# Performance work log

Hardware: AMD Instinct MI355X
Metric: run time of the kernel (lower is better)

## Reference

```python
import jax, jax.numpy as jnp
import numpy as np

B, L, D, F, K, M = 32, 1024, 384, 384, 3, 4096
LN_EPS = 1e-5


def setup_inputs() -> dict:
    key = jax.random.key(0)
    ks = jax.random.split(key, 6)
    w = lambda k, shp: jax.random.normal(k, shp, jnp.float32) * 0.02
    return {
        "x": jax.random.normal(ks[0], (B, L, D), jnp.float32),
        "target": jax.random.randint(ks[1], (B, L), 0, 5),
        "mel_max_length": M,
        "conv1_w": w(ks[2], (F, D, K)),  # OIW layout
        "conv1_b": jnp.zeros((F,), jnp.float32),
        "ln1_g": jnp.ones((F,), jnp.float32),
        "ln1_b": jnp.zeros((F,), jnp.float32),
        "conv2_w": w(ks[3], (F, F, K)),
        "conv2_b": jnp.zeros((F,), jnp.float32),
        "ln2_g": jnp.ones((F,), jnp.float32),
        "ln2_b": jnp.zeros((F,), jnp.float32),
        "lin_w": w(ks[4], (F, 1)),
        "lin_b": jnp.zeros((1,), jnp.float32),
    }


def conv1d_same(x, w, b):
    # x: [B, L, C], w: [O, I, K] -> [B, L, O], 'same' padding
    pad = (w.shape[-1] - 1) // 2
    y = jax.lax.conv_general_dilated(
        x, w, window_strides=(1,), padding=[(pad, pad)],
        dimension_numbers=("NWC", "OIW", "NWC"))
    return y + b


def layernorm(x, g, b):
    m = jnp.mean(x, axis=-1, keepdims=True)
    v = jnp.mean(jnp.square(x - m), axis=-1, keepdims=True)
    return (x - m) * jax.lax.rsqrt(v + LN_EPS) * g + b


def duration_predictor(x, c1w, c1b, g1, b1, c2w, c2b, g2, b2, lw, lb):
    h = jnp.maximum(layernorm(conv1d_same(x, c1w, c1b), g1, b1), 0.0)
    h = jnp.maximum(layernorm(conv1d_same(h, c2w, c2b), g2, b2), 0.0)
    return jnp.maximum(h @ lw + lb, 0.0)[..., 0]  # [B, L]


def length_regulate(x, durations, mel_max_length):
    # Equivalent to one-hot alignment matmul + zero pad, done as a gather.
    cum = jnp.cumsum(durations, axis=1)  # [B, L]
    t = jnp.arange(mel_max_length)       # [M]
    # frame t belongs to phoneme j where cum[j-1] <= t < cum[j]
    idx = jax.vmap(lambda c: jnp.searchsorted(c, t, side="right"))(cum)  # [B, M]
    valid = (t[None, :] < cum[:, -1:]).astype(x.dtype)                    # [B, M]
    idx = jnp.minimum(idx, durations.shape[1] - 1)
    out = jnp.take_along_axis(x, idx[..., None], axis=1) * valid[..., None]
    return out  # [B, M, D]


def reference(x, target, mel_max_length, conv1_w, conv1_b, ln1_g, ln1_b,
              conv2_w, conv2_b, ln2_g, ln2_b, lin_w, lin_b):
    dur_pred = duration_predictor(x, conv1_w, conv1_b, ln1_g, ln1_b,
                                  conv2_w, conv2_b, ln2_g, ln2_b, lin_w, lin_b)
    out = length_regulate(x, target, mel_max_length)
    return out, dur_pred
```

## Files before the change

kernel.cpp:

```cpp
#include <hip/hip_runtime.h>

#define DEV __device__ __forceinline__

typedef unsigned short u16;
typedef __attribute__((ext_vector_type(8))) short bf16x8;
typedef __attribute__((ext_vector_type(8))) unsigned short u16x8;
typedef __attribute__((ext_vector_type(4))) float f32x4;

constexpr int Bz = 32, Lz = 1024, Dz = 384, Fz = 384, KWz = 3, Mz = 4096;
constexpr float EPS = 1e-5f;

DEV u16 f2bf(float f) {
  unsigned u = __float_as_uint(f);
  u += 0x7fffu + ((u >> 16) & 1u);
  return (u16)(u >> 16);
}

typedef __attribute__((address_space(1))) const unsigned char ga_t;
typedef __attribute__((address_space(3))) unsigned char la_t;
DEV void gload16(const void* g, void* l) {
  __builtin_amdgcn_global_load_lds((ga_t*)g, (la_t*)l, 16, 0, 0);
}

__global__ void k_pre(const float* __restrict__ x, u16* __restrict__ xbf,
                      const float* __restrict__ w1, const float* __restrict__ w2,
                      u16* __restrict__ w1t, u16* __restrict__ w2t,
                      u16* __restrict__ h1) {
  constexpr int CONV_BLKS = (Bz * Lz * Dz / 8) / 256;
  if (blockIdx.x < CONV_BLKS) {
    int gid = blockIdx.x * 256 + threadIdx.x;
    size_t e = (size_t)gid * 8;
    float4 v0 = *reinterpret_cast<const float4*>(x + e);
    float4 v1 = *reinterpret_cast<const float4*>(x + e + 4);
    int d = (int)(e % Dz);
    int l = (int)((e / Dz) % Lz);
    int b = (int)(e / ((size_t)Dz * Lz));
    u16x8 u;
    u[0] = f2bf(v0.x); u[1] = f2bf(v0.y); u[2] = f2bf(v0.z); u[3] = f2bf(v0.w);
    u[4] = f2bf(v1.x); u[5] = f2bf(v1.y); u[6] = f2bf(v1.z); u[7] = f2bf(v1.w);
    *reinterpret_cast<u16x8*>(xbf + ((size_t)(b * (Lz + 2) + l + 1)) * Dz + d) = u;
    return;
  }
  int gid = (blockIdx.x - CONV_BLKS) * 256 + threadIdx.x;
  constexpr int WT = KWz * Fz * Dz;
  if (gid < WT) {
    int k = gid / (Fz * Dz), rem = gid % (Fz * Dz);
    int f = rem / Dz, d = rem % Dz;
    w1t[gid] = f2bf(w1[(f * Dz + d) * KWz + k]);
  } else if (gid < 2 * WT) {
    int g2 = gid - WT;
    int k = g2 / (Fz * Fz), rem = g2 % (Fz * Fz);
    int co = rem / Fz, ci = rem % Fz;
    w2t[g2] = f2bf(w2[(co * Fz + ci) * KWz + k]);
  } else {
    int p = gid - 2 * WT;
    if (p < 2 * Bz * 2 * Dz) {
      u16* buf = (p < Bz * 2 * Dz) ? xbf : h1;
      int q = p % (Bz * 2 * Dz);
      int b = q / (2 * Dz), r = (q / Dz) & 1, d = q % Dz;
      size_t row = (size_t)b * (Lz + 2) + (r ? (Lz + 1) : 0);
      buf[row * Dz + d] = 0;
    }
  }
}

__global__ __launch_bounds__(1024) void k_scan(const int* __restrict__ tgt,
                                               int* __restrict__ idxb) {
  __shared__ int sc[Lz];
  int b = blockIdx.x, tid = threadIdx.x;
  sc[tid] = tgt[b * Lz + tid];
  __syncthreads();
  for (int off = 1; off < Lz; off <<= 1) {
    int add = (tid >= off) ? sc[tid - off] : 0;
    __syncthreads();
    sc[tid] += add;
    __syncthreads();
  }
  int total = sc[Lz - 1];
  for (int t = tid; t < Mz; t += 1024) {
    int lo = 0, hi = Lz;
    while (lo < hi) {
      int mid = (lo + hi) >> 1;
      if (sc[mid] > t) hi = mid; else lo = mid + 1;
    }
    int iv = (t < total) ? (lo > Lz - 1 ? Lz - 1 : lo) : -1;
    idxb[b * Mz + t] = iv;
  }
}

__global__ void k_gather(const float* __restrict__ x, const int* __restrict__ idxb,
                         float* __restrict__ out) {
  int wid = (blockIdx.x * blockDim.x + threadIdx.x) >> 6;
  int lane = threadIdx.x & 63;
  int nw = (gridDim.x * blockDim.x) >> 6;
  for (int row = wid; row < Bz * Mz; row += nw) {
    int b = row >> 12;
    int iv = idxb[row];
    float4* dst = reinterpret_cast<float4*>(out + (size_t)row * Dz);
    if (iv < 0) {
      float4 z = make_float4(0.f, 0.f, 0.f, 0.f);
      dst[lane] = z;
      if (lane < 32) dst[64 + lane] = z;
    } else {
      const float4* src =
          reinterpret_cast<const float4*>(x + ((size_t)b * Lz + iv) * Dz);
      dst[lane] = src[lane];
      if (lane < 32) dst[64 + lane] = src[64 + lane];
    }
  }
}

template <int LAYER>
__global__ __launch_bounds__(512, 2) void k_conv(
    const u16* __restrict__ in,
    const u16* __restrict__ wt,
    const float* __restrict__ cbias,
    const float* __restrict__ lng, const float* __restrict__ lnb,
    u16* __restrict__ hout,
    const float* __restrict__ lw, const float* __restrict__ lbias,
    float* __restrict__ dur)
{
  __shared__ __align__(16) u16 Ash[3][128 * 32];
  __shared__ __align__(16) u16 Bsh[3][384 * 32];
  __shared__ float s_sum[4][128], s_sq[4][128], s_dot[4][128];

  const int tid = threadIdx.x;
  const int lane = tid & 63, wave = tid >> 6;
  const int wr = wave >> 2, wc = wave & 3;
  const int l15 = lane & 15, lh = lane >> 4;
  const int b = blockIdx.x >> 3, l0 = (blockIdx.x & 7) << 7;

  const u16* in_row = in + ((size_t)(b * (Lz + 2) + l0)) * 384;
  int gof[4], ldo[4];
  bool isa[4];
  #pragma unroll
  for (int i = 0; i < 4; ++i) {
    int c = wave + 8 * i;
    bool a = (c < 8);
    int cb = a ? c : c - 8;
    int slot = cb * 64 + lane, r = slot >> 2, q = slot & 3;
    int ks = q ^ ((r >> 1) & 3);
    gof[i] = r * 384 + ks * 8;
    ldo[i] = cb * 512;
    isa[i] = a;
  }

  auto STAGE = [&](int kt, int buf) {
    int tap = kt / 12;
    int d0 = (kt - tap * 12) * 32;
    const u16* sa = in_row + tap * 384 + d0;
    const u16* sb = wt + tap * (384 * 384) + d0;
    #pragma unroll
    for (int i = 0; i < 4; ++i) {
      if (isa[i]) gload16(sa + gof[i], &Ash[buf][ldo[i]]);
      else        gload16(sb + gof[i], &Bsh[buf][ldo[i]]);
    }
  };

  int aoff[4], boff[6];
  #pragma unroll
  for (int m = 0; m < 4; ++m) {
    int r = wr * 64 + m * 16 + l15;
    aoff[m] = r * 32 + (lh ^ ((r >> 1) & 3)) * 8;
  }
  #pragma unroll
  for (int n = 0; n < 6; ++n) {
    int c = wc * 96 + n * 16 + l15;
    boff[n] = c * 32 + (lh ^ ((c >> 1) & 3)) * 8;
  }

  f32x4 acc[4][6] = {};

  STAGE(0, 0);
  STAGE(1, 1);
  int cur = 0;
  for (int kt = 0; kt < 36; ++kt) {
    if (kt < 35) asm volatile("s_waitcnt vmcnt(4)" ::: "memory");
    else         asm volatile("s_waitcnt vmcnt(0)" ::: "memory");
    __builtin_amdgcn_s_barrier();
    __builtin_amdgcn_sched_barrier(0);
    bf16x8 av[4], bv[6];
    #pragma unroll
    for (int m = 0; m < 4; ++m)
      av[m] = *reinterpret_cast<const bf16x8*>(&Ash[cur][aoff[m]]);
    #pragma unroll
    for (int n = 0; n < 6; ++n)
      bv[n] = *reinterpret_cast<const bf16x8*>(&Bsh[cur][boff[n]]);
    if (kt < 34) {
      int nb = cur + 2; if (nb >= 3) nb -= 3;
      STAGE(kt + 2, nb);
    }
    #pragma unroll
    for (int m = 0; m < 4; ++m)
      #pragma unroll
      for (int n = 0; n < 6; ++n)
        acc[m][n] =
            __builtin_amdgcn_mfma_f32_16x16x32_bf16(av[m], bv[n], acc[m][n], 0, 0, 0);
    cur = (cur == 2) ? 0 : cur + 1;
  }

  __syncthreads();
  float gv[6], bvv[6], cbv[6], lwv[6];
  #pragma unroll
  for (int n = 0; n < 6; ++n) {
    int c = wc * 96 + n * 16 + l15;
    gv[n] = lng[c]; bvv[n] = lnb[c]; cbv[n] = cbias[c];
    lwv[n] = (LAYER == 2) ? lw[c] : 0.f;
  }
  #pragma unroll
  for (int m = 0; m < 4; ++m) {
    #pragma unroll
    for (int r = 0; r < 4; ++r) {
      float s = 0.f, q2 = 0.f;
      #pragma unroll
      for (int n = 0; n < 6; ++n) {
        float v = acc[m][n][r] + cbv[n];
        s += v; q2 += v * v;
      }
      #pragma unroll
      for (int off = 1; off < 16; off <<= 1) {
        s += __shfl_xor(s, off);
        q2 += __shfl_xor(q2, off);
      }
      if (l15 == 0) {
        int row = wr * 64 + m * 16 + lh * 4 + r;
        s_sum[wc][row] = s;
        s_sq[wc][row] = q2;
      }
    }
  }
  __syncthreads();
  #pragma unroll
  for (int m = 0; m < 4; ++m) {
    #pragma unroll
    for (int r = 0; r < 4; ++r) {
      int row = wr * 64 + m * 16 + lh * 4 + r;
      float S = 0.f, Q = 0.f;
      #pragma unroll
      for (int w = 0; w < 4; ++w) { S += s_sum[w][row]; Q += s_sq[w][row]; }
      float mean = S * (1.f / 384.f);
      float var = Q * (1.f / 384.f) - mean * mean;
      float rstd = rsqrtf(var + EPS);
      float dotp = 0.f;
      #pragma unroll
      for (int n = 0; n < 6; ++n) {
        float v = acc[m][n][r] + cbv[n];
        float y = fmaxf((v - mean) * rstd * gv[n] + bvv[n], 0.f);
        if constexpr (LAYER == 1) {
          int c = wc * 96 + n * 16 + l15;
          hout[((size_t)(b * (Lz + 2) + l0 + row + 1)) * 384 + c] = f2bf(y);
        } else {
          dotp += y * lwv[n];
        }
      }
      if constexpr (LAYER == 2) {
        #pragma unroll
        for (int off = 1; off < 16; off <<= 1) dotp += __shfl_xor(dotp, off);
        if (l15 == 0) s_dot[wc][row] = dotp;
      }
    }
  }
  if constexpr (LAYER == 2) {
    __syncthreads();
    if (tid < 128) {
      float dsum = lbias[0];
      #pragma unroll
      for (int w = 0; w < 4; ++w) dsum += s_dot[w][tid];
      dur[(size_t)b * Lz + l0 + tid] = fmaxf(dsum, 0.f);
    }
  }
}

extern "C" void kernel_launch(void* const* d_in, const int* in_sizes, int n_in,
                              void* d_out, int out_size, void* d_ws, size_t ws_size,
                              hipStream_t stream) {
  (void)in_sizes; (void)n_in; (void)out_size; (void)ws_size;
  const float* x   = (const float*)d_in[0];
  const int* tgt   = (const int*)d_in[1];
  const float* w1  = (const float*)d_in[3];
  const float* c1b = (const float*)d_in[4];
  const float* g1  = (const float*)d_in[5];
  const float* b1  = (const float*)d_in[6];
  const float* w2  = (const float*)d_in[7];
  const float* c2b = (const float*)d_in[8];
  const float* g2  = (const float*)d_in[9];
  const float* b2  = (const float*)d_in[10];
  const float* lw  = (const float*)d_in[11];
  const float* lb  = (const float*)d_in[12];

  float* out0 = (float*)d_out;
  float* dur  = out0 + (size_t)Bz * Mz * Dz;

  const size_t xbf_n = (size_t)Bz * (Lz + 2) * Dz;
  const size_t wt_n  = (size_t)KWz * Fz * Dz;
  u16* xbf = (u16*)d_ws;
  u16* h1  = xbf + xbf_n;
  u16* w1t = h1 + xbf_n;
  u16* w2t = w1t + wt_n;
  int* idxb = (int*)(w2t + wt_n);

  constexpr int CONV_BLKS = (Bz * Lz * Dz / 8) / 256;
  constexpr int PREP_BLKS = (2 * KWz * Fz * Dz + 2 * Bz * 2 * Dz + 255) / 256;
  k_pre<<<CONV_BLKS + PREP_BLKS, 256, 0, stream>>>(x, xbf, w1, w2, w1t, w2t, h1);
  k_scan<<<Bz, 1024, 0, stream>>>(tgt, idxb);
  k_conv<1><<<256, 512, 0, stream>>>(xbf, w1t, c1b, g1, b1, h1, nullptr, nullptr,
                                     nullptr);
  k_conv<2><<<256, 512, 0, stream>>>(h1, w2t, c2b, g2, b2, nullptr, lw, lb, dur);
  k_gather<<<2048, 256, 0, stream>>>(x, idxb, out0);
}
```

Measured before the change: 134.6 us.

## Fuse scan into prep kernel and overlap gather with conv via extra waves

Merges the cumsum/searchsorted scan into the preprocessing kernel as extra blocks and removes the standalone gather kernel. Each conv block gets four extra waves that copy half of the length-regulated output rows while the MFMA waves compute, matching their barriers to the conv's K-loop. The intent is to hide the memory-bound gather behind the compute-bound convolutions and cut launch count. The risk is that the extra waves and barrier matching alter occupancy (launch bounds 768,3), and any barrier-count mismatch with the unseen conv loop would hang or corrupt results.

```diff
diff --git a/kernel.cpp b/kernel.cpp
--- a/kernel.cpp
+++ b/kernel.cpp
@@ -22,13 +22,20 @@
   __builtin_amdgcn_global_load_lds((ga_t*)g, (la_t*)l, 16, 0, 0);
 }
 
-__global__ void k_pre(const float* __restrict__ x, u16* __restrict__ xbf,
-                      const float* __restrict__ w1, const float* __restrict__ w2,
-                      u16* __restrict__ w1t, u16* __restrict__ w2t,
-                      u16* __restrict__ h1) {
-  constexpr int CONV_BLKS = (Bz * Lz * Dz / 8) / 256;
+__global__ __launch_bounds__(1024) void k_pre(
+    const float* __restrict__ x, u16* __restrict__ xbf,
+    const float* __restrict__ w1, const float* __restrict__ w2,
+    u16* __restrict__ w1t, u16* __restrict__ w2t, u16* __restrict__ h1,
+    const int* __restrict__ tgt, int* __restrict__ idxb) {
+  __shared__ int sc[Lz];
+  constexpr int CONV_BLKS = (Bz * Lz * Dz / 8) / 1024;
+  constexpr int WT = KWz * Fz * Dz;
+  constexpr int PREP_ELEMS = 2 * WT + 2 * Bz * 2 * Dz;
+  constexpr int PREP_BLKS = (PREP_ELEMS + 1023) / 1024;
+  const int tid = threadIdx.x;
+
   if (blockIdx.x < CONV_BLKS) {
-    int gid = blockIdx.x * 256 + threadIdx.x;
+    int gid = blockIdx.x * 1024 + tid;
     size_t e = (size_t)gid * 8;
     float4 v0 = *reinterpret_cast<const float4*>(x + e);
     float4 v1 = *reinterpret_cast<const float4*>(x + e + 4);
@@ -41,33 +48,28 @@
     *reinterpret_cast<u16x8*>(xbf + ((size_t)(b * (Lz + 2) + l + 1)) * Dz + d) = u;
     return;
   }
-  int gid = (blockIdx.x - CONV_BLKS) * 256 + threadIdx.x;
-  constexpr int WT = KWz * Fz * Dz;
-  if (gid < WT) {
-    int k = gid / (Fz * Dz), rem = gid % (Fz * Dz);
-    int f = rem / Dz, d = rem % Dz;
-    w1t[gid] = f2bf(w1[(f * Dz + d) * KWz + k]);
-  } else if (gid < 2 * WT) {
-    int g2 = gid - WT;
-    int k = g2 / (Fz * Fz), rem = g2 % (Fz * Fz);
-    int co = rem / Fz, ci = rem % Fz;
-    w2t[g2] = f2bf(w2[(co * Fz + ci) * KWz + k]);
-  } else {
-    int p = gid - 2 * WT;
-    if (p < 2 * Bz * 2 * Dz) {
+  if (blockIdx.x < CONV_BLKS + PREP_BLKS) {
+    int gid = (blockIdx.x - CONV_BLKS) * 1024 + tid;
+    if (gid < WT) {
+      int k = gid / (Fz * Dz), rem = gid % (Fz * Dz);
+      int f = rem / Dz, d = rem % Dz;
+      w1t[gid] = f2bf(w1[(f * Dz + d) * KWz + k]);
+    } else if (gid < 2 * WT) {
+      int g2 = gid - WT;
+      int k = g2 / (Fz * Fz), rem = g2 % (Fz * Fz);
+      int co = rem / Fz, ci = rem % Fz;
+      w2t[g2] = f2bf(w2[(co * Fz + ci) * KWz + k]);
+    } else if (gid < PREP_ELEMS) {
+      int p = gid - 2 * WT;
       u16* buf = (p < Bz * 2 * Dz) ? xbf : h1;
       int q = p % (Bz * 2 * Dz);
       int b = q / (2 * Dz), r = (q / Dz) & 1, d = q % Dz;
       size_t row = (size_t)b * (Lz + 2) + (r ? (Lz + 1) : 0);
       buf[row * Dz + d] = 0;
     }
-  }
-}
-
-__global__ __launch_bounds__(1024) void k_scan(const int* __restrict__ tgt,
-                                               int* __restrict__ idxb) {
-  __shared__ int sc[Lz];
-  int b = blockIdx.x, tid = threadIdx.x;
+    return;
+  }
+  int b = blockIdx.x - CONV_BLKS - PREP_BLKS;
   sc[tid] = tgt[b * Lz + tid];
   __syncthreads();
   for (int off = 1; off < Lz; off <<= 1) {
@@ -88,37 +90,18 @@
   }
 }
 
-__global__ void k_gather(const float* __restrict__ x, const int* __restrict__ idxb,
-                         float* __restrict__ out) {
-  int wid = (blockIdx.x * blockDim.x + threadIdx.x) >> 6;
-  int lane = threadIdx.x & 63;
-  int nw = (gridDim.x * blockDim.x) >> 6;
-  for (int row = wid; row < Bz * Mz; row += nw) {
-    int b = row >> 12;
-    int iv = idxb[row];
-    float4* dst = reinterpret_cast<float4*>(out + (size_t)row * Dz);
-    if (iv < 0) {
-      float4 z = make_float4(0.f, 0.f, 0.f, 0.f);
-      dst[lane] = z;
-      if (lane < 32) dst[64 + lane] = z;
-    } else {
-      const float4* src =
-          reinterpret_cast<const float4*>(x + ((size_t)b * Lz + iv) * Dz);
-      dst[lane] = src[lane];
-      if (lane < 32) dst[64 + lane] = src[64 + lane];
-    }
-  }
-}
-
 template <int LAYER>
-__global__ __launch_bounds__(512, 2) void k_conv(
+__global__ __launch_bounds__(768, 3) void k_conv(
     const u16* __restrict__ in,
     const u16* __restrict__ wt,
     const float* __restrict__ cbias,
     const float* __restrict__ lng, const float* __restrict__ lnb,
     u16* __restrict__ hout,
     const float* __restrict__ lw, const float* __restrict__ lbias,
-    float* __restrict__ dur)
+    float* __restrict__ dur,
+    const float* __restrict__ xf,
+    const int* __restrict__ idxb,
+    float* __restrict__ out0)
 {
   __shared__ __align__(16) u16 Ash[3][128 * 32];
   __shared__ __align__(16) u16 Bsh[3][384 * 32];
@@ -126,9 +109,51 @@
 
   const int tid = threadIdx.x;
   const int lane = tid & 63, wave = tid >> 6;
-  const int wr = wave >> 2, wc = wave & 3;
   const int l15 = lane & 15, lh = lane >> 4;
   const int b = blockIdx.x >> 3, l0 = (blockIdx.x & 7) << 7;
+
+  if (wave >= 8) {
+    const int gw = wave - 8;
+    const int rbase = (LAYER == 1 ? 0 : (Bz * Mz) / 2) + blockIdx.x * 256 + gw * 64;
+    float4 ca0, cb0, ca1, cb1, na0, nb0, na1, nb1;
+    auto ldrow = [&](int row, float4& a, float4& bq) {
+      int iv = idxb[row];
+      if (iv < 0) {
+        a = make_float4(0.f, 0.f, 0.f, 0.f);
+        bq = a;
+      } else {
+        const float4* src =
+            reinterpret_cast<const float4*>(xf + ((size_t)(row >> 12) * Lz + iv) * Dz);
+        a = src[lane];
+        bq = (lane < 32) ? src[64 + lane] : a;
+      }
+    };
+    auto strow = [&](int row, float4 a, float4 bq) {
+      float4* dst = reinterpret_cast<float4*>(out0 + (size_t)row * Dz);
+      dst[lane] = a;
+      if (lane < 32) dst[64 + lane] = bq;
+    };
+    ldrow(rbase + 0, ca0, cb0);
+    ldrow(rbase + 1, ca1, cb1);
+    for (int kt = 0; kt < 36; ++kt) {
+      if (kt < 31) {
+        ldrow(rbase + 2 * (kt + 1), na0, nb0);
+        ldrow(rbase + 2 * (kt + 1) + 1, na1, nb1);
+      }
+      if (kt < 32) {
+        strow(rbase + 2 * kt, ca0, cb0);
+        strow(rbase + 2 * kt + 1, ca1, cb1);
+      }
+      ca0 = na0; cb0 = nb0; ca1 = na1; cb1 = nb1;
+      __builtin_amdgcn_s_barrier();
+    }
+    __builtin_amdgcn_s_barrier();
+    __builtin_amdgcn_s_barrier();
+    if constexpr (LAYER == 2) __builtin_amdgcn_s_barrier();
+    return;
+  }
+
+  const int wr = wave >> 2, wc = wave & 3;
 
   const u16* in_row = in + ((size_t)(b * (Lz + 2) + l0)) * 384;
   int gof[4], ldo[4];
@@ -299,12 +324,12 @@
   u16* w2t = w1t + wt_n;
   int* idxb = (int*)(w2t + wt_n);
 
-  constexpr int CONV_BLKS = (Bz * Lz * Dz / 8) / 256;
-  constexpr int PREP_BLKS = (2 * KWz * Fz * Dz + 2 * Bz * 2 * Dz + 255) / 256;
-  k_pre<<<CONV_BLKS + PREP_BLKS, 256, 0, stream>>>(x, xbf, w1, w2, w1t, w2t, h1);
-  k_scan<<<Bz, 1024, 0, stream>>>(tgt, idxb);
-  k_conv<1><<<256, 512, 0, stream>>>(xbf, w1t, c1b, g1, b1, h1, nullptr, nullptr,
-                                     nullptr);
-  k_conv<2><<<256, 512, 0, stream>>>(h1, w2t, c2b, g2, b2, nullptr, lw, lb, dur);
-  k_gather<<<2048, 256, 0, stream>>>(x, idxb, out0);
-}
+  constexpr int CONV_BLKS = (Bz * Lz * Dz / 8) / 1024;
+  constexpr int PREP_BLKS = (2 * KWz * Fz * Dz + 2 * Bz * 2 * Dz + 1023) / 1024;
+  k_pre<<<CONV_BLKS + PREP_BLKS + Bz, 1024, 0, stream>>>(x, xbf, w1, w2, w1t, w2t,
+                                                         h1, tgt, idxb);
+  k_conv<1><<<256, 768, 0, stream>>>(xbf, w1t, c1b, g1, b1, h1, nullptr, nullptr,
+                                     nullptr, x, idxb, out0);
+  k_conv<2><<<256, 768, 0, stream>>>(h1, w2t, c2b, g2, b2, nullptr, lw, lb, dur,
+                                     x, idxb, out0);
+}
```

New measurement: 180.7 us. 1.34x slower.

## Fuse fp32-to-bf16 input conversion into conv1 A-operand loads and merge scan into prep

Applied to the files above, without the earlier changes.

Removes the separate pass that converted x to a padded bf16 buffer. Conv1 now reads fp32 x straight into registers, handles the boundary padding by clamping and zeroing, and converts to bf16 before the MFMA. A operands are register-prefetched one step ahead, while weights are staged in a 4-deep LDS ring with vmcnt tuning. The scan kernel is folded into the prep kernel as extra blocks. This saves one full read and write of activations and one launch, but the A loads now skip LDS, so rows are re-read across column waves.

```diff
diff --git a/kernel.cpp b/kernel.cpp
--- a/kernel.cpp
+++ b/kernel.cpp
@@ -22,52 +22,38 @@
   __builtin_amdgcn_global_load_lds((ga_t*)g, (la_t*)l, 16, 0, 0);
 }
 
-__global__ void k_pre(const float* __restrict__ x, u16* __restrict__ xbf,
-                      const float* __restrict__ w1, const float* __restrict__ w2,
-                      u16* __restrict__ w1t, u16* __restrict__ w2t,
-                      u16* __restrict__ h1) {
-  constexpr int CONV_BLKS = (Bz * Lz * Dz / 8) / 256;
-  if (blockIdx.x < CONV_BLKS) {
-    int gid = blockIdx.x * 256 + threadIdx.x;
-    size_t e = (size_t)gid * 8;
-    float4 v0 = *reinterpret_cast<const float4*>(x + e);
-    float4 v1 = *reinterpret_cast<const float4*>(x + e + 4);
-    int d = (int)(e % Dz);
-    int l = (int)((e / Dz) % Lz);
-    int b = (int)(e / ((size_t)Dz * Lz));
-    u16x8 u;
-    u[0] = f2bf(v0.x); u[1] = f2bf(v0.y); u[2] = f2bf(v0.z); u[3] = f2bf(v0.w);
-    u[4] = f2bf(v1.x); u[5] = f2bf(v1.y); u[6] = f2bf(v1.z); u[7] = f2bf(v1.w);
-    *reinterpret_cast<u16x8*>(xbf + ((size_t)(b * (Lz + 2) + l + 1)) * Dz + d) = u;
+#define WAITV(n) asm volatile("s_waitcnt vmcnt(" #n ")" ::: "memory")
+
+__global__ __launch_bounds__(1024) void k_pre(
+    const float* __restrict__ w1, const float* __restrict__ w2,
+    u16* __restrict__ w1t, u16* __restrict__ w2t, u16* __restrict__ h1,
+    const int* __restrict__ tgt, int* __restrict__ idxb) {
+  __shared__ int sc[Lz];
+  constexpr int WT = KWz * Fz * Dz;
+  constexpr int PREP_ELEMS = 2 * WT + Bz * 2 * Dz;
+  constexpr int PREP_BLKS = (PREP_ELEMS + 1023) / 1024;
+  const int tid = threadIdx.x;
+
+  if (blockIdx.x < PREP_BLKS) {
+    int gid = blockIdx.x * 1024 + tid;
+    if (gid < WT) {
+      int k = gid / (Fz * Dz), rem = gid % (Fz * Dz);
+      int f = rem / Dz, d = rem % Dz;
+      w1t[gid] = f2bf(w1[(f * Dz + d) * KWz + k]);
+    } else if (gid < 2 * WT) {
+      int g2 = gid - WT;
+      int k = g2 / (Fz * Fz), rem = g2 % (Fz * Fz);
+      int co = rem / Fz, ci = rem % Fz;
+      w2t[g2] = f2bf(w2[(co * Fz + ci) * KWz + k]);
+    } else if (gid < PREP_ELEMS) {
+      int p = gid - 2 * WT;
+      int b = p / (2 * Dz), r = (p / Dz) & 1, d = p % Dz;
+      size_t row = (size_t)b * (Lz + 2) + (r ? (Lz + 1) : 0);
+      h1[row * Dz + d] = 0;
+    }
     return;
   }
-  int gid = (blockIdx.x - CONV_BLKS) * 256 + threadIdx.x;
-  constexpr int WT = KWz * Fz * Dz;
-  if (gid < WT) {
-    int k = gid / (Fz * Dz), rem = gid % (Fz * Dz);
-    int f = rem / Dz, d = rem % Dz;
-    w1t[gid] = f2bf(w1[(f * Dz + d) * KWz + k]);
-  } else if (gid < 2 * WT) {
-    int g2 = gid - WT;
-    int k = g2 / (Fz * Fz), rem = g2 % (Fz * Fz);
-    int co = rem / Fz, ci = rem % Fz;
-    w2t[g2] = f2bf(w2[(co * Fz + ci) * KWz + k]);
-  } else {
-    int p = gid - 2 * WT;
-    if (p < 2 * Bz * 2 * Dz) {
-      u16* buf = (p < Bz * 2 * Dz) ? xbf : h1;
-      int q = p % (Bz * 2 * Dz);
-      int b = q / (2 * Dz), r = (q / Dz) & 1, d = q % Dz;
-      size_t row = (size_t)b * (Lz + 2) + (r ? (Lz + 1) : 0);
-      buf[row * Dz + d] = 0;
-    }
-  }
-}
-
-__global__ __launch_bounds__(1024) void k_scan(const int* __restrict__ tgt,
-                                               int* __restrict__ idxb) {
-  __shared__ int sc[Lz];
-  int b = blockIdx.x, tid = threadIdx.x;
+  int b = blockIdx.x - PREP_BLKS;
   sc[tid] = tgt[b * Lz + tid];
   __syncthreads();
   for (int off = 1; off < Lz; off <<= 1) {
@@ -112,7 +98,7 @@
 
 template <int LAYER>
 __global__ __launch_bounds__(512, 2) void k_conv(
-    const u16* __restrict__ in,
+    const void* __restrict__ Asrc,
     const u16* __restrict__ wt,
     const float* __restrict__ cbias,
     const float* __restrict__ lng, const float* __restrict__ lnb,
@@ -120,49 +106,68 @@
     const float* __restrict__ lw, const float* __restrict__ lbias,
     float* __restrict__ dur)
 {
-  __shared__ __align__(16) u16 Ash[3][128 * 32];
-  __shared__ __align__(16) u16 Bsh[3][384 * 32];
+  __shared__ __align__(16) u16 Bsh[4][384 * 32];
   __shared__ float s_sum[4][128], s_sq[4][128], s_dot[4][128];
 
   const int tid = threadIdx.x;
   const int lane = tid & 63, wave = tid >> 6;
   const int wr = wave >> 2, wc = wave & 3;
   const int l15 = lane & 15, lh = lane >> 4;
+  const int lh8 = lh * 8;
   const int b = blockIdx.x >> 3, l0 = (blockIdx.x & 7) << 7;
 
-  const u16* in_row = in + ((size_t)(b * (Lz + 2) + l0)) * 384;
-  int gof[4], ldo[4];
-  bool isa[4];
-  #pragma unroll
-  for (int i = 0; i < 4; ++i) {
+  int gof[3], ldo[3];
+  #pragma unroll
+  for (int i = 0; i < 3; ++i) {
     int c = wave + 8 * i;
-    bool a = (c < 8);
-    int cb = a ? c : c - 8;
-    int slot = cb * 64 + lane, r = slot >> 2, q = slot & 3;
-    int ks = q ^ ((r >> 1) & 3);
-    gof[i] = r * 384 + ks * 8;
-    ldo[i] = cb * 512;
-    isa[i] = a;
-  }
-
+    int slot = c * 64 + lane, f = slot >> 2, q = slot & 3;
+    int ks = q ^ ((f >> 1) & 3);
+    gof[i] = f * 384 + ks * 8;
+    ldo[i] = c * 512;
+  }
   auto STAGE = [&](int kt, int buf) {
     int tap = kt / 12;
     int d0 = (kt - tap * 12) * 32;
-    const u16* sa = in_row + tap * 384 + d0;
     const u16* sb = wt + tap * (384 * 384) + d0;
     #pragma unroll
-    for (int i = 0; i < 4; ++i) {
-      if (isa[i]) gload16(sa + gof[i], &Ash[buf][ldo[i]]);
-      else        gload16(sb + gof[i], &Bsh[buf][ldo[i]]);
-    }
+    for (int i = 0; i < 3; ++i) gload16(sb + gof[i], &Bsh[buf][ldo[i]]);
   };
 
-  int aoff[4], boff[6];
+  const float* xb = (const float*)Asrc + (size_t)b * Lz * 384;
+  int arow[4];
+  const u16* Pm[4];
   #pragma unroll
   for (int m = 0; m < 4; ++m) {
-    int r = wr * 64 + m * 16 + l15;
-    aoff[m] = r * 32 + (lh ^ ((r >> 1) & 3)) * 8;
-  }
+    int rel = wr * 64 + m * 16 + l15;
+    arow[m] = l0 + rel;
+    Pm[m] = (const u16*)Asrc +
+            ((size_t)(b * (Lz + 2) + l0 + rel)) * 384 + lh8;
+  }
+  float4 pLo[2][4], pHi[2][4];
+  bf16x8 pB[2][4];
+
+  auto AISSUE1 = [&](int kt, float4 (&lo)[4], float4 (&hi)[4]) {
+    int tap = kt / 12, d0 = (kt - tap * 12) * 32;
+    #pragma unroll
+    for (int m = 0; m < 4; ++m) {
+      int q = arow[m] + tap - 1;
+      int qc = q < 0 ? 0 : (q > Lz - 1 ? Lz - 1 : q);
+      const float* p = xb + (size_t)qc * 384 + d0 + lh8;
+      float4 a = *reinterpret_cast<const float4*>(p);
+      float4 c = *reinterpret_cast<const float4*>(p + 4);
+      if (q != qc) { a = make_float4(0.f, 0.f, 0.f, 0.f); c = a; }
+      lo[m] = a; hi[m] = c;
+    }
+  };
+  auto AISSUE2 = [&](int kt, bf16x8 (&pb)[4]) {
+    int tap = kt / 12, d0 = (kt - tap * 12) * 32;
+    int off = tap * 384 + d0;
+    #pragma unroll
+    for (int m = 0; m < 4; ++m)
+      pb[m] = *reinterpret_cast<const bf16x8*>(Pm[m] + off);
+  };
+
+  int boff[6];
   #pragma unroll
   for (int n = 0; n < 6; ++n) {
     int c = wc * 96 + n * 16 + l15;
@@ -173,31 +178,58 @@
 
   STAGE(0, 0);
   STAGE(1, 1);
-  int cur = 0;
-  for (int kt = 0; kt < 36; ++kt) {
-    if (kt < 35) asm volatile("s_waitcnt vmcnt(4)" ::: "memory");
-    else         asm volatile("s_waitcnt vmcnt(0)" ::: "memory");
-    __builtin_amdgcn_s_barrier();
-    __builtin_amdgcn_sched_barrier(0);
-    bf16x8 av[4], bv[6];
-    #pragma unroll
-    for (int m = 0; m < 4; ++m)
-      av[m] = *reinterpret_cast<const bf16x8*>(&Ash[cur][aoff[m]]);
-    #pragma unroll
-    for (int n = 0; n < 6; ++n)
-      bv[n] = *reinterpret_cast<const bf16x8*>(&Bsh[cur][boff[n]]);
-    if (kt < 34) {
-      int nb = cur + 2; if (nb >= 3) nb -= 3;
-      STAGE(kt + 2, nb);
-    }
-    #pragma unroll
-    for (int m = 0; m < 4; ++m)
-      #pragma unroll
-      for (int n = 0; n < 6; ++n)
-        acc[m][n] =
-            __builtin_amdgcn_mfma_f32_16x16x32_bf16(av[m], bv[n], acc[m][n], 0, 0, 0);
-    cur = (cur == 2) ? 0 : cur + 1;
-  }
+  if constexpr (LAYER == 1) AISSUE1(0, pLo[0], pHi[0]);
+  else                      AISSUE2(0, pB[0]);
+  STAGE(2, 2);
+
+#define PHASE(KT, U, V)                                                        \
+  {                                                                            \
+    const int kt = (KT);                                                       \
+    if constexpr (LAYER == 1) {                                                \
+      if (kt < 34) WAITV(14); else if (kt == 34) WAITV(11); else WAITV(8);     \
+    } else {                                                                   \
+      if (kt < 34) WAITV(10); else if (kt == 34) WAITV(7); else WAITV(4);      \
+    }                                                                          \
+    __builtin_amdgcn_s_barrier();                                              \
+    __builtin_amdgcn_sched_barrier(0);                                         \
+    if (kt < 35) {                                                             \
+      if constexpr (LAYER == 1) AISSUE1(kt + 1, pLo[V], pHi[V]);               \
+      else                      AISSUE2(kt + 1, pB[V]);                        \
+    }                                                                          \
+    if (kt <= 32) STAGE(kt + 3, (kt + 3) & 3);                                 \
+    __builtin_amdgcn_sched_barrier(0);                                         \
+    bf16x8 av[4];                                                              \
+    if constexpr (LAYER == 1) {                                                \
+      _Pragma("unroll")                                                        \
+      for (int m = 0; m < 4; ++m) {                                            \
+        u16x8 f;                                                               \
+        f[0] = f2bf(pLo[U][m].x); f[1] = f2bf(pLo[U][m].y);                    \
+        f[2] = f2bf(pLo[U][m].z); f[3] = f2bf(pLo[U][m].w);                    \
+        f[4] = f2bf(pHi[U][m].x); f[5] = f2bf(pHi[U][m].y);                    \
+        f[6] = f2bf(pHi[U][m].z); f[7] = f2bf(pHi[U][m].w);                    \
+        av[m] = (bf16x8)f;                                                     \
+      }                                                                        \
+    } else {                                                                   \
+      _Pragma("unroll")                                                        \
+      for (int m = 0; m < 4; ++m) av[m] = pB[U][m];                            \
+    }                                                                          \
+    bf16x8 bv[6];                                                              \
+    _Pragma("unroll")                                                          \
+    for (int n = 0; n < 6; ++n)                                                \
+      bv[n] = *reinterpret_cast<const bf16x8*>(&Bsh[kt & 3][boff[n]]);         \
+    _Pragma("unroll")                                                          \
+    for (int m = 0; m < 4; ++m)                                                \
+      _Pragma("unroll")                                                        \
+      for (int n = 0; n < 6; ++n)                                              \
+        acc[m][n] = __builtin_amdgcn_mfma_f32_16x16x32_bf16(av[m], bv[n],      \
+                                                            acc[m][n], 0, 0, 0);\
+  }
+
+  for (int k2 = 0; k2 < 18; ++k2) {
+    PHASE(2 * k2, 0, 1);
+    PHASE(2 * k2 + 1, 1, 0);
+  }
+#undef PHASE
 
   __syncthreads();
   float gv[6], bvv[6], cbv[6], lwv[6];
@@ -291,19 +323,17 @@
   float* out0 = (float*)d_out;
   float* dur  = out0 + (size_t)Bz * Mz * Dz;
 
-  const size_t xbf_n = (size_t)Bz * (Lz + 2) * Dz;
-  const size_t wt_n  = (size_t)KWz * Fz * Dz;
-  u16* xbf = (u16*)d_ws;
-  u16* h1  = xbf + xbf_n;
-  u16* w1t = h1 + xbf_n;
+  const size_t h1_n = (size_t)Bz * (Lz + 2) * Dz;
+  const size_t wt_n = (size_t)KWz * Fz * Dz;
+  u16* h1  = (u16*)d_ws;
+  u16* w1t = h1 + h1_n;
   u16* w2t = w1t + wt_n;
   int* idxb = (int*)(w2t + wt_n);
 
-  constexpr int CONV_BLKS = (Bz * Lz * Dz / 8) / 256;
-  constexpr int PREP_BLKS = (2 * KWz * Fz * Dz + 2 * Bz * 2 * Dz + 255) / 256;
-  k_pre<<<CONV_BLKS + PREP_BLKS, 256, 0, stream>>>(x, xbf, w1, w2, w1t, w2t, h1);
-  k_scan<<<Bz, 1024, 0, stream>>>(tgt, idxb);
-  k_conv<1><<<256, 512, 0, stream>>>(xbf, w1t, c1b, g1, b1, h1, nullptr, nullptr,
+  constexpr int PREP_BLKS =
+      (2 * KWz * Fz * Dz + Bz * 2 * Dz + 1023) / 1024;
+  k_pre<<<PREP_BLKS + Bz, 1024, 0, stream>>>(w1, w2, w1t, w2t, h1, tgt, idxb);
+  k_conv<1><<<256, 512, 0, stream>>>(x, w1t, c1b, g1, b1, h1, nullptr, nullptr,
                                      nullptr);
   k_conv<2><<<256, 512, 0, stream>>>(h1, w2t, c2b, g2, b2, nullptr, lw, lb, dur);
   k_gather<<<2048, 256, 0, stream>>>(x, idxb, out0);
```

Result: slower. 222.3 us (+65.2%).

## Fuse fp32-to-bf16 input conversion into conv1 loads and merge prep with scan

Applied to the files above, without the earlier changes.

Conv layer 1 now stages fp32 rows of x straight into LDS with clamped row indices, then converts them to bf16 in registers and zeroes the padding rows. This removes the separate padded bf16 copy of x and the global write and read that came with it. The weight prep and cumsum/searchsorted scan are also merged into one launch. The cost is double the LDS for the A tile, conversion work repeated across the three taps, and extra VALU work inside the MFMA loop.

```diff
diff --git a/kernel.cpp b/kernel.cpp
--- a/kernel.cpp
+++ b/kernel.cpp
@@ -22,52 +22,36 @@
   __builtin_amdgcn_global_load_lds((ga_t*)g, (la_t*)l, 16, 0, 0);
 }
 
-__global__ void k_pre(const float* __restrict__ x, u16* __restrict__ xbf,
-                      const float* __restrict__ w1, const float* __restrict__ w2,
-                      u16* __restrict__ w1t, u16* __restrict__ w2t,
-                      u16* __restrict__ h1) {
-  constexpr int CONV_BLKS = (Bz * Lz * Dz / 8) / 256;
-  if (blockIdx.x < CONV_BLKS) {
-    int gid = blockIdx.x * 256 + threadIdx.x;
-    size_t e = (size_t)gid * 8;
-    float4 v0 = *reinterpret_cast<const float4*>(x + e);
-    float4 v1 = *reinterpret_cast<const float4*>(x + e + 4);
-    int d = (int)(e % Dz);
-    int l = (int)((e / Dz) % Lz);
-    int b = (int)(e / ((size_t)Dz * Lz));
-    u16x8 u;
-    u[0] = f2bf(v0.x); u[1] = f2bf(v0.y); u[2] = f2bf(v0.z); u[3] = f2bf(v0.w);
-    u[4] = f2bf(v1.x); u[5] = f2bf(v1.y); u[6] = f2bf(v1.z); u[7] = f2bf(v1.w);
-    *reinterpret_cast<u16x8*>(xbf + ((size_t)(b * (Lz + 2) + l + 1)) * Dz + d) = u;
+__global__ __launch_bounds__(1024) void k_pre(
+    const float* __restrict__ w1, const float* __restrict__ w2,
+    u16* __restrict__ w1t, u16* __restrict__ w2t, u16* __restrict__ h1,
+    const int* __restrict__ tgt, int* __restrict__ idxb) {
+  __shared__ int sc[Lz];
+  constexpr int WT = KWz * Fz * Dz;
+  constexpr int PREP_ELEMS = 2 * WT + Bz * 2 * Dz;
+  constexpr int PREP_BLKS = (PREP_ELEMS + 1023) / 1024;
+  const int tid = threadIdx.x;
+
+  if (blockIdx.x < PREP_BLKS) {
+    int gid = blockIdx.x * 1024 + tid;
+    if (gid < WT) {
+      int k = gid / (Fz * Dz), rem = gid % (Fz * Dz);
+      int f = rem / Dz, d = rem % Dz;
+      w1t[gid] = f2bf(w1[(f * Dz + d) * KWz + k]);
+    } else if (gid < 2 * WT) {
+      int g2 = gid - WT;
+      int k = g2 / (Fz * Fz), rem = g2 % (Fz * Fz);
+      int co = rem / Fz, ci = rem % Fz;
+      w2t[g2] = f2bf(w2[(co * Fz + ci) * KWz + k]);
+    } else if (gid < PREP_ELEMS) {
+      int p = gid - 2 * WT;
+      int b = p / (2 * Dz), r = (p / Dz) & 1, d = p % Dz;
+      size_t row = (size_t)b * (Lz + 2) + (r ? (Lz + 1) : 0);
+      h1[row * Dz + d] = 0;
+    }
     return;
   }
-  int gid = (blockIdx.x - CONV_BLKS) * 256 + threadIdx.x;
-  constexpr int WT = KWz * Fz * Dz;
-  if (gid < WT) {
-    int k = gid / (Fz * Dz), rem = gid % (Fz * Dz);
-    int f = rem / Dz, d = rem % Dz;
-    w1t[gid] = f2bf(w1[(f * Dz + d) * KWz + k]);
-  } else if (gid < 2 * WT) {
-    int g2 = gid - WT;
-    int k = g2 / (Fz * Fz), rem = g2 % (Fz * Fz);
-    int co = rem / Fz, ci = rem % Fz;
-    w2t[g2] = f2bf(w2[(co * Fz + ci) * KWz + k]);
-  } else {
-    int p = gid - 2 * WT;
-    if (p < 2 * Bz * 2 * Dz) {
-      u16* buf = (p < Bz * 2 * Dz) ? xbf : h1;
-      int q = p % (Bz * 2 * Dz);
-      int b = q / (2 * Dz), r = (q / Dz) & 1, d = q % Dz;
-      size_t row = (size_t)b * (Lz + 2) + (r ? (Lz + 1) : 0);
-      buf[row * Dz + d] = 0;
-    }
-  }
-}
-
-__global__ __launch_bounds__(1024) void k_scan(const int* __restrict__ tgt,
-                                               int* __restrict__ idxb) {
-  __shared__ int sc[Lz];
-  int b = blockIdx.x, tid = threadIdx.x;
+  int b = blockIdx.x - PREP_BLKS;
   sc[tid] = tgt[b * Lz + tid];
   __syncthreads();
   for (int off = 1; off < Lz; off <<= 1) {
@@ -112,7 +96,7 @@
 
 template <int LAYER>
 __global__ __launch_bounds__(512, 2) void k_conv(
-    const u16* __restrict__ in,
+    const void* __restrict__ Asrc,
     const u16* __restrict__ wt,
     const float* __restrict__ cbias,
     const float* __restrict__ lng, const float* __restrict__ lnb,
@@ -120,7 +104,8 @@
     const float* __restrict__ lw, const float* __restrict__ lbias,
     float* __restrict__ dur)
 {
-  __shared__ __align__(16) u16 Ash[3][128 * 32];
+  constexpr int ABYTES = (LAYER == 1) ? 16384 : 8192;
+  __shared__ __align__(16) unsigned char Ash[3][ABYTES];
   __shared__ __align__(16) u16 Bsh[3][384 * 32];
   __shared__ float s_sum[4][128], s_sq[4][128], s_dot[4][128];
 
@@ -130,39 +115,67 @@
   const int l15 = lane & 15, lh = lane >> 4;
   const int b = blockIdx.x >> 3, l0 = (blockIdx.x & 7) << 7;
 
-  const u16* in_row = in + ((size_t)(b * (Lz + 2) + l0)) * 384;
-  int gof[4], ldo[4];
-  bool isa[4];
-  #pragma unroll
-  for (int i = 0; i < 4; ++i) {
+  int bgof[3], bldo[3];
+  #pragma unroll
+  for (int i = 0; i < 3; ++i) {
     int c = wave + 8 * i;
-    bool a = (c < 8);
-    int cb = a ? c : c - 8;
-    int slot = cb * 64 + lane, r = slot >> 2, q = slot & 3;
+    int slot = c * 64 + lane, f = slot >> 2, q = slot & 3;
+    int ks = q ^ ((f >> 1) & 3);
+    bgof[i] = f * 384 + ks * 8;
+    bldo[i] = c * 512;
+  }
+
+  const float* xb = (const float*)Asrc + (size_t)b * Lz * 384;
+  const u16* in_row =
+      (const u16*)Asrc + ((size_t)(b * (Lz + 2) + l0)) * 384;
+  int a_row[2], a_gcol[2], a_ldsb[2];
+  int a_gof = 0, a_ldo = 0;
+  if constexpr (LAYER == 1) {
+    #pragma unroll
+    for (int i = 0; i < 2; ++i) {
+      int c = wave + 8 * i;
+      int s = c * 64 + lane;
+      int row = s >> 3, q = s & 7, p = q >> 1, e = q & 1;
+      int pp = p ^ (row & 3);
+      a_row[i] = row;
+      a_gcol[i] = pp * 8 + e * 4;
+      a_ldsb[i] = c * 1024;
+    }
+  } else {
+    int c = wave;
+    int slot = c * 64 + lane, r = slot >> 2, q = slot & 3;
     int ks = q ^ ((r >> 1) & 3);
-    gof[i] = r * 384 + ks * 8;
-    ldo[i] = cb * 512;
-    isa[i] = a;
+    a_gof = r * 384 + ks * 8;
+    a_ldo = c * 1024;
   }
 
   auto STAGE = [&](int kt, int buf) {
     int tap = kt / 12;
     int d0 = (kt - tap * 12) * 32;
-    const u16* sa = in_row + tap * 384 + d0;
     const u16* sb = wt + tap * (384 * 384) + d0;
     #pragma unroll
-    for (int i = 0; i < 4; ++i) {
-      if (isa[i]) gload16(sa + gof[i], &Ash[buf][ldo[i]]);
-      else        gload16(sb + gof[i], &Bsh[buf][ldo[i]]);
+    for (int i = 0; i < 3; ++i) gload16(sb + bgof[i], &Bsh[buf][bldo[i]]);
+    if constexpr (LAYER == 1) {
+      #pragma unroll
+      for (int i = 0; i < 2; ++i) {
+        int grow = l0 + a_row[i] + tap - 1;
+        grow = grow < 0 ? 0 : (grow > Lz - 1 ? Lz - 1 : grow);
+        gload16(xb + (size_t)grow * 384 + d0 + a_gcol[i],
+                &Ash[buf][a_ldsb[i]]);
+      }
+    } else {
+      gload16(in_row + tap * 384 + d0 + a_gof, &Ash[buf][a_ldo]);
     }
   };
 
-  int aoff[4], boff[6];
+  int tr[4];
+  int aoff2[4];
   #pragma unroll
   for (int m = 0; m < 4; ++m) {
-    int r = wr * 64 + m * 16 + l15;
-    aoff[m] = r * 32 + (lh ^ ((r >> 1) & 3)) * 8;
-  }
+    tr[m] = wr * 64 + m * 16 + l15;
+    aoff2[m] = tr[m] * 32 + (lh ^ ((tr[m] >> 1) & 3)) * 8;
+  }
+  int boff[6];
   #pragma unroll
   for (int n = 0; n < 6; ++n) {
     int c = wc * 96 + n * 16 + l15;
@@ -175,14 +188,38 @@
   STAGE(1, 1);
   int cur = 0;
   for (int kt = 0; kt < 36; ++kt) {
-    if (kt < 35) asm volatile("s_waitcnt vmcnt(4)" ::: "memory");
-    else         asm volatile("s_waitcnt vmcnt(0)" ::: "memory");
+    if constexpr (LAYER == 1) {
+      if (kt < 35) asm volatile("s_waitcnt vmcnt(5)" ::: "memory");
+      else         asm volatile("s_waitcnt vmcnt(0)" ::: "memory");
+    } else {
+      if (kt < 35) asm volatile("s_waitcnt vmcnt(4)" ::: "memory");
+      else         asm volatile("s_waitcnt vmcnt(0)" ::: "memory");
+    }
     __builtin_amdgcn_s_barrier();
     __builtin_amdgcn_sched_barrier(0);
+    const int tap = kt / 12;
     bf16x8 av[4], bv[6];
-    #pragma unroll
-    for (int m = 0; m < 4; ++m)
-      av[m] = *reinterpret_cast<const bf16x8*>(&Ash[cur][aoff[m]]);
+    if constexpr (LAYER == 1) {
+      const float* af = (const float*)Ash[cur];
+      #pragma unroll
+      for (int m = 0; m < 4; ++m) {
+        int fidx = tr[m] * 32 + (lh ^ (tr[m] & 3)) * 8;
+        float4 lo = *reinterpret_cast<const float4*>(af + fidx);
+        float4 hi = *reinterpret_cast<const float4*>(af + fidx + 4);
+        int grow = l0 + tr[m] + tap - 1;
+        bool oob = (unsigned)grow > (unsigned)(Lz - 1);
+        u16x8 f;
+        f[0] = f2bf(lo.x); f[1] = f2bf(lo.y); f[2] = f2bf(lo.z); f[3] = f2bf(lo.w);
+        f[4] = f2bf(hi.x); f[5] = f2bf(hi.y); f[6] = f2bf(hi.z); f[7] = f2bf(hi.w);
+        if (oob) f = (u16x8)(unsigned short)0;
+        av[m] = (bf16x8)f;
+      }
+    } else {
+      const u16* au = (const u16*)Ash[cur];
+      #pragma unroll
+      for (int m = 0; m < 4; ++m)
+        av[m] = *reinterpret_cast<const bf16x8*>(au + aoff2[m]);
+    }
     #pragma unroll
     for (int n = 0; n < 6; ++n)
       bv[n] = *reinterpret_cast<const bf16x8*>(&Bsh[cur][boff[n]]);
@@ -291,19 +328,17 @@
   float* out0 = (float*)d_out;
   float* dur  = out0 + (size_t)Bz * Mz * Dz;
 
-  const size_t xbf_n = (size_t)Bz * (Lz + 2) * Dz;
-  const size_t wt_n  = (size_t)KWz * Fz * Dz;
-  u16* xbf = (u16*)d_ws;
-  u16* h1  = xbf + xbf_n;
-  u16* w1t = h1 + xbf_n;
+  const size_t h1_n = (size_t)Bz * (Lz + 2) * Dz;
+  const size_t wt_n = (size_t)KWz * Fz * Dz;
+  u16* h1  = (u16*)d_ws;
+  u16* w1t = h1 + h1_n;
   u16* w2t = w1t + wt_n;
   int* idxb = (int*)(w2t + wt_n);
 
-  constexpr int CONV_BLKS = (Bz * Lz * Dz / 8) / 256;
-  constexpr int PREP_BLKS = (2 * KWz * Fz * Dz + 2 * Bz * 2 * Dz + 255) / 256;
-  k_pre<<<CONV_BLKS + PREP_BLKS, 256, 0, stream>>>(x, xbf, w1, w2, w1t, w2t, h1);
-  k_scan<<<Bz, 1024, 0, stream>>>(tgt, idxb);
-  k_conv<1><<<256, 512, 0, stream>>>(xbf, w1t, c1b, g1, b1, h1, nullptr, nullptr,
+  constexpr int PREP_BLKS =
+      (2 * KWz * Fz * Dz + Bz * 2 * Dz + 1023) / 1024;
+  k_pre<<<PREP_BLKS + Bz, 1024, 0, stream>>>(w1, w2, w1t, w2t, h1, tgt, idxb);
+  k_conv<1><<<256, 512, 0, stream>>>(x, w1t, c1b, g1, b1, h1, nullptr, nullptr,
                                      nullptr);
   k_conv<2><<<256, 512, 0, stream>>>(h1, w2t, c2b, g2, b2, nullptr, lw, lb, dur);
   k_gather<<<2048, 256, 0, stream>>>(x, idxb, out0);
```

Result: faster. 130.3 us (-3.2%).
